# Performance work log

Measured on AMD Instinct MI355X. Metric: run time of the kernel, lower is better.

Reference implementation:

```python
import jax, jax.numpy as jnp
import numpy as np

B, C_EDGE, C_FUSED, C_SEM = 4, 64, 128, 128
H = W = 64
MASK_SIZE = 11
EPS = 1e-6


def _window_mask(h, w, mask_size):
    # M_dw: 0 inside the clipped (mask_size x mask_size) window around each query pixel, -10000 outside.
    half = mask_size // 2
    idx = jnp.arange(h * w)
    qx, qy = idx // w, idx % w
    inside = (jnp.abs(qx[:, None] - qx[None, :]) <= half) & (jnp.abs(qy[:, None] - qy[None, :]) <= half)
    return jnp.where(inside, 0.0, -10000.0).astype(jnp.float32)


def _conv1x1(x, w, b):
    # x: [b, cin, h, w], w: [cout, cin]
    return jnp.einsum('bchw,oc->bohw', x, w) + b[None, :, None, None]


def _proj1d(x, w, b):
    # x: [b, cin, n], w: [cout, cin]
    return jnp.einsum('bcn,oc->bon', x, w) + b[None, :, None]


def _bilinear(x, h, w):
    # matches F.interpolate(mode='bilinear', align_corners=False)
    b, c = x.shape[0], x.shape[1]
    return jax.image.resize(x, (b, c, h, w), method='linear', antialias=False)


def setup_inputs() -> dict:
    key = jax.random.key(0)
    ks = jax.random.split(key, 13)
    s = 0.05
    return {
        'edge_features': jax.random.normal(ks[0], (B, C_EDGE, 32, 32), jnp.float32),
        'semantic_features': jax.random.normal(ks[1], (B, C_SEM, H, W), jnp.float32),
        'fused_features': jax.random.normal(ks[2], (B, C_FUSED, 32, 32), jnp.float32),
        'w_align': jax.random.normal(ks[3], (C_SEM, C_EDGE), jnp.float32) * s,
        'b_align': jax.random.normal(ks[4], (C_SEM,), jnp.float32) * s,
        'w_fused_align': jax.random.normal(ks[5], (C_SEM, C_FUSED), jnp.float32) * s,
        'b_fused_align': jax.random.normal(ks[6], (C_SEM,), jnp.float32) * s,
        'w_q': jax.random.normal(ks[7], (2 * C_SEM, 2 * C_SEM), jnp.float32) * s,
        'b_q': jax.random.normal(ks[8], (2 * C_SEM,), jnp.float32) * s,
        'w_k': jax.random.normal(ks[9], (2 * C_SEM, 2 * C_SEM), jnp.float32) * s,
        'b_k': jax.random.normal(ks[10], (2 * C_SEM,), jnp.float32) * s,
        'w_fusion': jax.random.normal(ks[11], (C_SEM, 2 * C_SEM), jnp.float32) * s,
        'b_fusion': jax.random.normal(ks[12], (C_SEM,), jnp.float32) * s,
    }


def reference(edge_features, semantic_features, fused_features,
              w_align, b_align, w_fused_align, b_fused_align,
              w_q, b_q, w_k, b_k, w_fusion, b_fusion):
    b, c, h, w = semantic_features.shape
    n = h * w

    edge = _conv1x1(_bilinear(edge_features, h, w), w_align, b_align)            # [b,c,h,w]
    fused = _conv1x1(_bilinear(fused_features, h, w), w_fused_align, b_fused_align)

    l2_edge = jnp.sqrt(jnp.sum(edge * edge, axis=1, keepdims=True))              # [b,1,h,w]
    l2_sem = jnp.sqrt(jnp.sum(semantic_features * semantic_features, axis=1, keepdims=True))
    similarity = jnp.sum((edge / (l2_edge + EPS)) * (semantic_features / (l2_sem + EPS)),
                         axis=1, keepdims=True)
    similarity = (similarity + 1.0) * 0.5

    density_flat = l2_edge.reshape(b, n)
    density = (jax.nn.softmax(density_flat, axis=1) * n).reshape(b, 1, h, w)

    edge_t = (edge * similarity).reshape(b, c, n)
    sem_t = (semantic_features * density).reshape(b, c, n)
    fused_t = fused.reshape(b, c, n)
    sem_raw = semantic_features.reshape(b, c, n)

    edge_cat = jnp.concatenate([edge_t, edge_t], axis=1)    # [b,2c,n]
    sem_cat = jnp.concatenate([sem_t, fused_t], axis=1)
    sem_val = jnp.concatenate([sem_raw, fused_t], axis=1)

    q = _proj1d(edge_cat, w_q, b_q)                          # [b,2c,n]
    k = _proj1d(sem_cat, w_k, b_k)

    scale = 1.0 / jnp.sqrt(jnp.float32(2 * c))
    attn = jnp.einsum('bcn,bcm->bnm', q, k) * scale          # [b,n,n]
    attn = attn + _window_mask(h, w, MASK_SIZE)
    attn = jax.nn.softmax(attn, axis=-1)

    out = jnp.einsum('bnm,bcm->bnc', attn, sem_val)          # [b,n,2c]
    out = out.reshape(b, h, w, 2 * c).transpose(0, 3, 1, 2)  # [b,2c,h,w]
    return _conv1x1(out, w_fusion, b_fusion)
```

## Files before the change

### kernel.cpp

```cpp
#include <hip/hip_runtime.h>
#include <hip/hip_bf16.h>

#define NB 4
#define C 128
#define N 4096
#define EPS 1e-6f
#define PW 80
#define PIMG 5120

typedef float f32x4 __attribute__((ext_vector_type(4)));
typedef short bf16x8 __attribute__((ext_vector_type(8)));
typedef unsigned short ushort_t;
typedef unsigned int uint_t;

__device__ __forceinline__ ushort_t f2bf(float f) {
  __hip_bfloat16 h = __float2bfloat16(f);
  return *reinterpret_cast<ushort_t*>(&h);
}

struct alignas(8) us4 { ushort_t a, b, c, d; };

__device__ __forceinline__ void conv_body(const float* __restrict__ x,
                                          const float* __restrict__ w,
                                          const float* __restrict__ bias,
                                          float* __restrict__ out,
                                          int n, int o0, int b, int CIN) {
  const float* xb = x + (size_t)(b * CIN) * 1024 + n;
  float a0 = 0.f, a1 = 0.f, a2 = 0.f, a3 = 0.f;
  for (int c = 0; c < CIN; ++c) {
    float xv = xb[(size_t)c * 1024];
    a0 += w[(o0 + 0) * CIN + c] * xv;
    a1 += w[(o0 + 1) * CIN + c] * xv;
    a2 += w[(o0 + 2) * CIN + c] * xv;
    a3 += w[(o0 + 3) * CIN + c] * xv;
  }
  size_t ob = ((size_t)b * 128 + o0) * 1024 + n;
  out[ob]        = a0 + bias[o0];
  out[ob + 1024] = a1 + bias[o0 + 1];
  out[ob + 2048] = a2 + bias[o0 + 2];
  out[ob + 3072] = a3 + bias[o0 + 3];
}

__global__ void prep_misc(const float* __restrict__ edge_f, const float* __restrict__ w_align,
                          const float* __restrict__ b_align,
                          const float* __restrict__ fused_f, const float* __restrict__ w_fal,
                          const float* __restrict__ b_fal,
                          const float* __restrict__ wq, const float* __restrict__ wk,
                          const float* __restrict__ wf,
                          ushort_t* __restrict__ wqf, ushort_t* __restrict__ wkf,
                          ushort_t* __restrict__ wff,
                          float* __restrict__ edge32, float* __restrict__ fused32,
                          float* __restrict__ dsum) {
  int bx = blockIdx.x, t = threadIdx.x;
  if (bx < 64) {
    if (bx == 0 && t < NB) dsum[t] = 0.f;
    int c = bx * 256 + t;
    int lane = c & 63;
    int mrow = lane & 15, quad = lane >> 4;
    if (c < 4096) {
      int grp = c >> 6;
      int tile = grp >> 2, kslot = grp & 3;
      int o = tile * 16 + mrow, k0 = kslot * 32 + quad * 8;
      const float* s = wq + o * 256 + k0;
      ushort_t* d = wqf + (size_t)c * 8;
#pragma unroll
      for (int j = 0; j < 8; ++j) d[j] = f2bf(s[j] + s[128 + j]);
    } else if (c < 12288) {
      int c2 = c - 4096;
      int grp = c2 >> 6;
      int tile = grp >> 3, kslot = grp & 7;
      int o = tile * 16 + mrow, k0 = kslot * 32 + quad * 8;
      const float* s = wk + o * 256 + k0;
      ushort_t* d = wkf + (size_t)c2 * 8;
#pragma unroll
      for (int j = 0; j < 8; ++j) d[j] = f2bf(s[j]);
    } else {
      int c2 = c - 12288;
      int grp = c2 >> 6;
      int tile = grp >> 3, kslot = grp & 7;
      int o = tile * 16 + mrow, k0 = kslot * 32 + quad * 8;
      const float* s = wf + o * 256 + k0;
      ushort_t* d = wff + (size_t)c2 * 8;
#pragma unroll
      for (int j = 0; j < 8; ++j) d[j] = f2bf(s[j]);
    }
  } else if (bx < 576) {
    int j = bx - 64;
    conv_body(edge_f, w_align, b_align, edge32, (j & 3) * 256 + t, ((j >> 2) & 31) * 4, j >> 7, 64);
  } else {
    int j = bx - 576;
    conv_body(fused_f, w_fal, b_fal, fused32, (j & 3) * 256 + t, ((j >> 2) & 31) * 4, j >> 7, 128);
  }
}

__global__ __launch_bounds__(256) void prep_acts(const float* __restrict__ edge32,
                                                 const float* __restrict__ fused32,
                                                 const float* __restrict__ sem,
                                                 const ushort_t* __restrict__ wqf,
                                                 const ushort_t* __restrict__ wff,
                                                 const float* __restrict__ b_q,
                                                 ushort_t* __restrict__ xt_sem,
                                                 ushort_t* __restrict__ xt_fused,
                                                 float* __restrict__ simb,
                                                 float* __restrict__ l2e,
                                                 float* __restrict__ dsum,
                                                 ushort_t* __restrict__ qtb,
                                                 ushort_t* __restrict__ v2b) {
  int b = blockIdx.y, bx = blockIdx.x;
  int y = bx >> 1, xh = (bx & 1) * 32;
  int t = threadIdx.x;
  int nl = t & 31, cg = t >> 5;
  int x = xh + nl;
  int yy0 = (y & 1) ? (y >> 1) : (y >> 1) - 1;
  float fy = (y & 1) ? 0.25f : 0.75f;
  int y0c = max(yy0, 0), y1c = min(yy0 + 1, 31);
  int xx0 = (x & 1) ? (x >> 1) : (x >> 1) - 1;
  float fx = (x & 1) ? 0.25f : 0.75f;
  int x0c = max(xx0, 0), x1c = min(xx0 + 1, 31);

  __shared__ uint_t se[32][68], ssm[32][68], sf[32][68];
  __shared__ float red[4][3][32];
  __shared__ float simL[32];
  __shared__ ushort_t vstg[128 * 40];

  float ee = 0.f, ssum = 0.f, es = 0.f;
#pragma unroll 2
  for (int p = 0; p < 8; ++p) {
    float evs[2], fvs[2], svs[2];
#pragma unroll
    for (int u = 0; u < 2; ++u) {
      int c = cg * 16 + p * 2 + u;
      const float* ip = edge32 + ((size_t)(b * 128 + c)) * 1024;
      float e00 = ip[y0c * 32 + x0c], e01 = ip[y0c * 32 + x1c];
      float e10 = ip[y1c * 32 + x0c], e11 = ip[y1c * 32 + x1c];
      float ev = (1.f - fy) * ((1.f - fx) * e00 + fx * e01) + fy * ((1.f - fx) * e10 + fx * e11);
      const float* fp = fused32 + ((size_t)(b * 128 + c)) * 1024;
      float f00 = fp[y0c * 32 + x0c], f01 = fp[y0c * 32 + x1c];
      float f10 = fp[y1c * 32 + x0c], f11 = fp[y1c * 32 + x1c];
      float fv = (1.f - fy) * ((1.f - fx) * f00 + fx * f01) + fy * ((1.f - fx) * f10 + fx * f11);
      float sv = sem[((size_t)(b * 128 + c)) * 4096 + y * 64 + x];
      ee += ev * ev; ssum += sv * sv; es += ev * sv;
      evs[u] = ev; fvs[u] = fv; svs[u] = sv;
    }
    int col = cg * 8 + p;
    se[nl][col]  = (uint_t)f2bf(evs[0]) | ((uint_t)f2bf(evs[1]) << 16);
    sf[nl][col]  = (uint_t)f2bf(fvs[0]) | ((uint_t)f2bf(fvs[1]) << 16);
    ssm[nl][col] = (uint_t)f2bf(svs[0]) | ((uint_t)f2bf(svs[1]) << 16);
  }
  ee += __shfl_xor(ee, 32, 64); ssum += __shfl_xor(ssum, 32, 64); es += __shfl_xor(es, 32, 64);
  int w = t >> 6, lane = t & 63;
  int l15 = lane & 15, quad = lane >> 4;
  if (lane < 32) { red[w][0][lane] = ee; red[w][1][lane] = ssum; red[w][2][lane] = es; }
  __syncthreads();

  int base_n = b * 4096 + y * 64 + xh;
#pragma unroll
  for (int rep = 0; rep < 8; ++rep) {
    int d = rep * 256 + t;
    int r = d >> 6, cp = d & 63;
    ((uint_t*)xt_sem)[(size_t)(base_n + r) * 64 + cp] = ssm[r][cp];
    ((uint_t*)xt_fused)[(size_t)(base_n + r) * 64 + cp] = sf[r][cp];
  }
  if (t < 32) {
    float E = 0.f, S = 0.f, X = 0.f;
#pragma unroll
    for (int w2 = 0; w2 < 4; ++w2) { E += red[w2][0][t]; S += red[w2][1][t]; X += red[w2][2][t]; }
    float le = sqrtf(E), ls = sqrtf(S);
    float sv = (X / ((le + EPS) * (ls + EPS)) + 1.f) * 0.5f;
    simb[base_n + t] = sv;
    simL[t] = sv;
    l2e[base_n + t] = le;
    float pe = expf(le - 16.f);
#pragma unroll
    for (int m2 = 16; m2; m2 >>= 1) pe += __shfl_xor(pe, m2, 64);
    if (t == 0) atomicAdd(&dsum[b], pe);
  }
  __syncthreads();

#pragma unroll
  for (int h = 0; h < 2; ++h) {
    f32x4 vacc[2];
    vacc[0] = (f32x4){0.f,0.f,0.f,0.f};
    vacc[1] = (f32x4){0.f,0.f,0.f,0.f};
#pragma unroll
    for (int kk = 0; kk < 4; ++kk) {
      bf16x8 bfr = *(const bf16x8*)&ssm[h * 16 + l15][kk * 16 + quad * 4];
#pragma unroll
      for (int i = 0; i < 2; ++i) {
        bf16x8 afr = *(const bf16x8*)(wff + (size_t)(((w + i * 4) * 8 + kk) * 64 + lane) * 8);
        vacc[i] = __builtin_amdgcn_mfma_f32_16x16x32_bf16(afr, bfr, vacc[i], 0, 0, 0);
      }
    }
#pragma unroll
    for (int kk = 0; kk < 4; ++kk) {
      bf16x8 bfr = *(const bf16x8*)&sf[h * 16 + l15][kk * 16 + quad * 4];
#pragma unroll
      for (int i = 0; i < 2; ++i) {
        bf16x8 afr = *(const bf16x8*)(wff + (size_t)(((w + i * 4) * 8 + 4 + kk) * 64 + lane) * 8);
        vacc[i] = __builtin_amdgcn_mfma_f32_16x16x32_bf16(afr, bfr, vacc[i], 0, 0, 0);
      }
    }
#pragma unroll
    for (int i = 0; i < 2; ++i) {
#pragma unroll
      for (int r = 0; r < 4; ++r) {
        int ch = (w + i * 4) * 16 + quad * 4 + r;
        vstg[ch * 40 + h * 16 + l15] = f2bf(vacc[i][r]);
      }
    }
  }

#pragma unroll
  for (int h = 0; h < 2; ++h) {
    f32x4 qacc[4];
#pragma unroll
    for (int i = 0; i < 4; ++i) qacc[i] = (f32x4){0.f,0.f,0.f,0.f};
#pragma unroll
    for (int kk = 0; kk < 4; ++kk) {
      bf16x8 bfr = *(const bf16x8*)&se[h * 16 + l15][kk * 16 + quad * 4];
#pragma unroll
      for (int i = 0; i < 4; ++i) {
        bf16x8 afr = *(const bf16x8*)(wqf + (size_t)(((w * 4 + i) * 4 + kk) * 64 + lane) * 8);
        qacc[i] = __builtin_amdgcn_mfma_f32_16x16x32_bf16(afr, bfr, qacc[i], 0, 0, 0);
      }
    }
    int px = h * 16 + l15;
    float sv = simL[px];
    int n = y * 64 + xh + px;
#pragma unroll
    for (int i = 0; i < 4; ++i) {
      int o = (w * 4 + i) * 16 + quad * 4;
      float4 bq = *(const float4*)(b_q + o);
      us4 pk = { f2bf(sv * qacc[i][0] + bq.x), f2bf(sv * qacc[i][1] + bq.y),
                 f2bf(sv * qacc[i][2] + bq.z), f2bf(sv * qacc[i][3] + bq.w) };
      *(us4*)(qtb + ((size_t)b * N + n) * 256 + o) = pk;
    }
  }

  __syncthreads();
  int np0 = y * PW + 8 + xh;
#pragma unroll
  for (int r2 = 0; r2 < 2; ++r2) {
    int idx = r2 * 256 + t;
    int ch = idx >> 2, seg = idx & 3;
    *(bf16x8*)(v2b + ((size_t)b * 128 + ch) * PIMG + np0 + seg * 8) =
        *(const bf16x8*)&vstg[ch * 40 + seg * 8];
  }
}

__global__ __launch_bounds__(256) void gemm_k(const ushort_t* __restrict__ xt_sem,
                                              const ushort_t* __restrict__ xt_fused,
                                              const ushort_t* __restrict__ wkf,
                                              const float* __restrict__ b_k,
                                              const float* __restrict__ l2e,
                                              const float* __restrict__ dsum,
                                              ushort_t* __restrict__ ktb) {
  int y = blockIdx.x, bI = blockIdx.y;
  int t = threadIdx.x, w = t >> 6, lane = t & 63;
  int mrow = lane & 15, quad = lane >> 4;
  __shared__ __align__(16) ushort_t stg[16896];

  int n0 = y * 64, o0 = w * 64;
  float dscale = 4096.f / dsum[bI];
  for (int nt = 0; nt < 4; ++nt) {
    int n0t = n0 + nt * 16;
    const ushort_t* bS = xt_sem + ((size_t)bI * N + n0t + mrow) * 128 + quad * 8;
    const ushort_t* bF = xt_fused + ((size_t)bI * N + n0t + mrow) * 128 + quad * 8;
    f32x4 accL[4], accR[4];
#pragma unroll
    for (int i = 0; i < 4; ++i) { accL[i] = (f32x4){0.f,0.f,0.f,0.f}; accR[i] = (f32x4){0.f,0.f,0.f,0.f}; }
#pragma unroll
    for (int kk = 0; kk < 4; ++kk) {
      bf16x8 bfr = *(const bf16x8*)(bS + kk * 32);
#pragma unroll
      for (int i = 0; i < 4; ++i) {
        bf16x8 afr = *(const bf16x8*)(wkf + (size_t)((((w * 4 + i) * 8) + kk) * 64 + lane) * 8);
        accL[i] = __builtin_amdgcn_mfma_f32_16x16x32_bf16(afr, bfr, accL[i], 0, 0, 0);
      }
    }
#pragma unroll
    for (int kk = 0; kk < 4; ++kk) {
      bf16x8 bfr = *(const bf16x8*)(bF + kk * 32);
#pragma unroll
      for (int i = 0; i < 4; ++i) {
        bf16x8 afr = *(const bf16x8*)(wkf + (size_t)((((w * 4 + i) * 8) + 4 + kk) * 64 + lane) * 8);
        accR[i] = __builtin_amdgcn_mfma_f32_16x16x32_bf16(afr, bfr, accR[i], 0, 0, 0);
      }
    }
    int n = n0t + mrow;
    float dv = expf(l2e[bI * N + n] - 16.f) * dscale;
#pragma unroll
    for (int i = 0; i < 4; ++i) {
      int o = o0 + i * 16 + quad * 4;
      float4 bk = *(const float4*)(b_k + o);
      us4 pk = { f2bf(accL[i][0] * dv + accR[i][0] + bk.x),
                 f2bf(accL[i][1] * dv + accR[i][1] + bk.y),
                 f2bf(accL[i][2] * dv + accR[i][2] + bk.z),
                 f2bf(accL[i][3] * dv + accR[i][3] + bk.w) };
      *(us4*)&stg[(nt * 16 + mrow) * 264 + o] = pk;
    }
  }
  __syncthreads();
  int np0 = y * PW + 8;
#pragma unroll
  for (int r = 0; r < 8; ++r) {
    int cidx = r * 256 + t;
    int row = cidx >> 5, cc = cidx & 31;
    *(bf16x8*)(ktb + ((size_t)bI * PIMG + np0 + row) * 256 + cc * 8) =
        *(const bf16x8*)&stg[row * 264 + cc * 8];
  }
}

__global__ __launch_bounds__(256) void attn_kernel(const ushort_t* __restrict__ qtb,
                                                   const ushort_t* __restrict__ ktb,
                                                   const ushort_t* __restrict__ v2b,
                                                   const float* __restrict__ b_fusion,
                                                   float* __restrict__ out) {
  int L = blockIdx.x;
  int xcd = L & 7, j = L >> 3;
  int b = xcd >> 1;
  int ty0 = (((xcd & 1) << 3) + (j >> 3)) * 4;
  int tx0 = (j & 7) * 8;
  int y0 = max(ty0 - 5, 0), y1 = min(ty0 + 8, 63);
  int nh = y1 - y0 + 1;
  int x0a = tx0 - 8, cb = tx0;
  int ntq = (nh * 3 + 1) >> 1;
  int npv = (nh * 3 + 3) >> 2;

  __shared__ ushort_t pst[32][352];
  __shared__ float redm[4][2][16], reds[4][2][16];

  int t = threadIdx.x, w = t >> 6, lane = t & 63;
  int l15 = lane & 15, quad = lane >> 4;

  int gap = npv * 32 - ntq * 16;
  for (int idx = t; idx < 32 * gap; idx += 256)
    pst[idx & 31][ntq * 16 + (idx >> 5)] = 0;

  int n_s0 = (ty0 + (l15 >> 3)) * 64 + tx0 + (l15 & 7);
  int n_s1 = n_s0 + 128;
  bf16x8 qfr[2][8];
  {
    const ushort_t* q0 = qtb + ((size_t)b * N + n_s0) * 256 + quad * 8;
    const ushort_t* q1 = qtb + ((size_t)b * N + n_s1) * 256 + quad * 8;
#pragma unroll
    for (int ks = 0; ks < 8; ++ks) {
      qfr[0][ks] = *(const bf16x8*)(q0 + ks * 32);
      qfr[1][ks] = *(const bf16x8*)(q1 + ks * 32);
    }
  }
  int qx = tx0 + (l15 & 7);
  int qy0 = ty0 + (l15 >> 3);

  const ushort_t* kb = ktb + (size_t)b * PIMG * 256;
  f32x4 sc[6][2];
#pragma unroll
  for (int i = 0; i < 6; ++i) {
    int tq = w + i * 4;
    if (tq >= ntq) break;
    int key = tq * 16 + l15;
    int ry = (key * 2731) >> 16;
    int rx = key - ry * 24;
    int yy = min(y0 + ry, 63);
    const ushort_t* krow = kb + (size_t)(yy * PW + cb + rx) * 256 + quad * 8;
    f32x4 a0 = (f32x4){0.f,0.f,0.f,0.f}, a1 = (f32x4){0.f,0.f,0.f,0.f};
#pragma unroll
    for (int ks = 0; ks < 8; ++ks) {
      bf16x8 afr = *(const bf16x8*)(krow + ks * 32);
      a0 = __builtin_amdgcn_mfma_f32_16x16x32_bf16(afr, qfr[0][ks], a0, 0, 0, 0);
      a1 = __builtin_amdgcn_mfma_f32_16x16x32_bf16(afr, qfr[1][ks], a1, 0, 0, 0);
    }
    sc[i][0] = a0; sc[i][1] = a1;
  }
  float mymax0 = -1e30f, mymax1 = -1e30f;
#pragma unroll
  for (int i = 0; i < 6; ++i) {
    int tq = w + i * 4;
    if (tq >= ntq) break;
#pragma unroll
    for (int r = 0; r < 4; ++r) {
      int key = tq * 16 + quad * 4 + r;
      int ry = (key * 2731) >> 16;
      int rx = key - ry * 24;
      int x = x0a + rx;
      int dx = x - qx;
      bool xok = (dx >= -5) && (dx <= 5) && (x >= 0) && (x <= 63) && (ry < nh);
      int dy0 = y0 + ry - qy0;
      float s0 = (xok && dy0 >= -5 && dy0 <= 5) ? sc[i][0][r] * 0.0625f : -1e30f;
      int dy1 = dy0 - 2;
      float s1 = (xok && dy1 >= -5 && dy1 <= 5) ? sc[i][1][r] * 0.0625f : -1e30f;
      sc[i][0][r] = s0; sc[i][1][r] = s1;
      mymax0 = fmaxf(mymax0, s0); mymax1 = fmaxf(mymax1, s1);
    }
  }
  mymax0 = fmaxf(mymax0, __shfl_xor(mymax0, 16, 64));
  mymax0 = fmaxf(mymax0, __shfl_xor(mymax0, 32, 64));
  mymax1 = fmaxf(mymax1, __shfl_xor(mymax1, 16, 64));
  mymax1 = fmaxf(mymax1, __shfl_xor(mymax1, 32, 64));
  if (quad == 0) { redm[w][0][l15] = mymax0; redm[w][1][l15] = mymax1; }
  __syncthreads();
  float gmax0 = fmaxf(fmaxf(redm[0][0][l15], redm[1][0][l15]), fmaxf(redm[2][0][l15], redm[3][0][l15]));
  float gmax1 = fmaxf(fmaxf(redm[0][1][l15], redm[1][1][l15]), fmaxf(redm[2][1][l15], redm[3][1][l15]));
  float mysum0 = 0.f, mysum1 = 0.f;
#pragma unroll
  for (int i = 0; i < 6; ++i) {
    int tq = w + i * 4;
    if (tq >= ntq) break;
#pragma unroll
    for (int r = 0; r < 4; ++r) {
      float e0 = expf(sc[i][0][r] - gmax0);
      float e1 = expf(sc[i][1][r] - gmax1);
      sc[i][0][r] = e0; sc[i][1][r] = e1;
      mysum0 += e0; mysum1 += e1;
    }
  }
  mysum0 += __shfl_xor(mysum0, 16, 64); mysum0 += __shfl_xor(mysum0, 32, 64);
  mysum1 += __shfl_xor(mysum1, 16, 64); mysum1 += __shfl_xor(mysum1, 32, 64);
  if (quad == 0) { reds[w][0][l15] = mysum0; reds[w][1][l15] = mysum1; }
#pragma unroll
  for (int i = 0; i < 6; ++i) {
    int tq = w + i * 4;
    if (tq >= ntq) break;
    int kc = tq * 16 + quad * 4;
#pragma unroll
    for (int s = 0; s < 2; ++s) {
      uint_t p01 = (uint_t)f2bf(sc[i][s][0]) | ((uint_t)f2bf(sc[i][s][1]) << 16);
      uint_t p23 = (uint_t)f2bf(sc[i][s][2]) | ((uint_t)f2bf(sc[i][s][3]) << 16);
      *(uint_t*)(&pst[s * 16 + l15][kc]) = p01;
      *(uint_t*)(&pst[s * 16 + l15][kc + 2]) = p23;
    }
  }
  __syncthreads();

  float rinv0 = 1.f / (reds[0][0][l15] + reds[1][0][l15] + reds[2][0][l15] + reds[3][0][l15]);
  float rinv1 = 1.f / (reds[0][1][l15] + reds[1][1][l15] + reds[2][1][l15] + reds[3][1][l15]);

  const ushort_t* vb = v2b + (size_t)b * 128 * PIMG;
#pragma unroll
  for (int half = 0; half < 2; ++half) {
    int ch0 = half * 64 + w * 16;
    const ushort_t* vrow = vb + (size_t)(ch0 + l15) * PIMG;
    f32x4 acc0 = (f32x4){0.f,0.f,0.f,0.f}, acc1 = (f32x4){0.f,0.f,0.f,0.f};
    for (int ks = 0; ks < npv; ++ks) {
      int kst = ks * 32 + quad * 8;
      int ry = (kst * 2731) >> 16;
      int rxs = kst - ry * 24;
      int yy = min(y0 + ry, 63);
      bf16x8 av = *(const bf16x8*)(vrow + yy * PW + cb + rxs);
      bf16x8 bp0 = *(const bf16x8*)(&pst[l15][kst]);
      bf16x8 bp1 = *(const bf16x8*)(&pst[16 + l15][kst]);
      acc0 = __builtin_amdgcn_mfma_f32_16x16x32_bf16(av, bp0, acc0, 0, 0, 0);
      acc1 = __builtin_amdgcn_mfma_f32_16x16x32_bf16(av, bp1, acc1, 0, 0, 0);
    }
    int chg = ch0 + quad * 4;
    float4 bf4 = *(const float4*)(b_fusion + chg);
    float bfa[4] = {bf4.x, bf4.y, bf4.z, bf4.w};
#pragma unroll
    for (int r = 0; r < 4; ++r) {
      out[((size_t)b * 128 + chg + r) * N + n_s0] = acc0[r] * rinv0 + bfa[r];
      out[((size_t)b * 128 + chg + r) * N + n_s1] = acc1[r] * rinv1 + bfa[r];
    }
  }
}

extern "C" void kernel_launch(void* const* d_in, const int* in_sizes, int n_in,
                              void* d_out, int out_size, void* d_ws, size_t ws_size,
                              hipStream_t stream) {
  (void)in_sizes; (void)n_in; (void)out_size; (void)ws_size;
  const float* edge_f  = (const float*)d_in[0];
  const float* sem     = (const float*)d_in[1];
  const float* fused_f = (const float*)d_in[2];
  const float* w_align = (const float*)d_in[3];
  const float* b_align = (const float*)d_in[4];
  const float* w_fal   = (const float*)d_in[5];
  const float* b_fal   = (const float*)d_in[6];
  const float* w_q     = (const float*)d_in[7];
  const float* b_q     = (const float*)d_in[8];
  const float* w_k     = (const float*)d_in[9];
  const float* b_k     = (const float*)d_in[10];
  const float* w_fus   = (const float*)d_in[11];
  const float* b_fus   = (const float*)d_in[12];
  float* out = (float*)d_out;

  float* ws = (float*)d_ws;
  float* edge32   = ws;
  float* fused32  = ws + 524288;
  float* simb     = ws + 1048576;
  float* l2e      = ws + 1064960;
  float* dsum     = ws + 1081344;
  ushort_t* xt_sem   = (ushort_t*)(ws + 1097728);
  ushort_t* xt_fused = (ushort_t*)(ws + 2146304);
  ushort_t* wqf      = (ushort_t*)(ws + 3194880);
  ushort_t* wkf      = (ushort_t*)(ws + 3211264);
  ushort_t* wff      = (ushort_t*)(ws + 3244032);
  ushort_t* qtb      = (ushort_t*)(ws + 3260416);
  ushort_t* ktb      = (ushort_t*)(ws + 5357568);
  ushort_t* v2b      = (ushort_t*)(ws + 7979008);

  prep_misc<<<1088, 256, 0, stream>>>(edge_f, w_align, b_align, fused_f, w_fal, b_fal,
                                      w_q, w_k, w_fus, wqf, wkf, wff, edge32, fused32, dsum);
  prep_acts<<<dim3(128, NB), 256, 0, stream>>>(edge32, fused32, sem, wqf, wff, b_q,
                                               xt_sem, xt_fused, simb, l2e, dsum, qtb, v2b);
  gemm_k<<<dim3(64, NB), 256, 0, stream>>>(xt_sem, xt_fused, wkf, b_k, l2e, dsum, ktb);
  attn_kernel<<<512, 256, 0, stream>>>(qtb, ktb, v2b, b_fus, out);
}
```

Measured before the change: 159.6 us.

## Double prep_acts threads per block and split gemm_k into 16-row blocks

prep_acts now runs 512 threads per block, so each wave handles half the channels, one V tile and two Q tiles. The cross-wave reduction buffer grows to eight entries to match. gemm_k launches four times as many blocks, each computing 16 pixels instead of looping over 64, with a smaller shared staging buffer. Both changes aim to raise parallelism and occupancy on the memory-bound preparation stages, at the cost of more blocks and less weight reuse per block.

After: 159.6 us. Within noise of the previous version (+0.0%).

```diff
diff --git a/kernel.cpp b/kernel.cpp
--- a/kernel.cpp
+++ b/kernel.cpp
@@ -93,19 +93,19 @@
   }
 }
 
-__global__ __launch_bounds__(256) void prep_acts(const float* __restrict__ edge32,
-                                                 const float* __restrict__ fused32,
-                                                 const float* __restrict__ sem,
-                                                 const ushort_t* __restrict__ wqf,
-                                                 const ushort_t* __restrict__ wff,
-                                                 const float* __restrict__ b_q,
-                                                 ushort_t* __restrict__ xt_sem,
-                                                 ushort_t* __restrict__ xt_fused,
-                                                 float* __restrict__ simb,
-                                                 float* __restrict__ l2e,
-                                                 float* __restrict__ dsum,
-                                                 ushort_t* __restrict__ qtb,
-                                                 ushort_t* __restrict__ v2b) {
+__global__ __launch_bounds__(512, 4) void prep_acts(const float* __restrict__ edge32,
+                                                    const float* __restrict__ fused32,
+                                                    const float* __restrict__ sem,
+                                                    const ushort_t* __restrict__ wqf,
+                                                    const ushort_t* __restrict__ wff,
+                                                    const float* __restrict__ b_q,
+                                                    ushort_t* __restrict__ xt_sem,
+                                                    ushort_t* __restrict__ xt_fused,
+                                                    float* __restrict__ simb,
+                                                    float* __restrict__ l2e,
+                                                    float* __restrict__ dsum,
+                                                    ushort_t* __restrict__ qtb,
+                                                    ushort_t* __restrict__ v2b) {
   int b = blockIdx.y, bx = blockIdx.x;
   int y = bx >> 1, xh = (bx & 1) * 32;
   int t = threadIdx.x;
@@ -119,17 +119,17 @@
   int x0c = max(xx0, 0), x1c = min(xx0 + 1, 31);
 
   __shared__ uint_t se[32][68], ssm[32][68], sf[32][68];
-  __shared__ float red[4][3][32];
+  __shared__ float red[8][3][32];
   __shared__ float simL[32];
   __shared__ ushort_t vstg[128 * 40];
 
   float ee = 0.f, ssum = 0.f, es = 0.f;
 #pragma unroll 2
-  for (int p = 0; p < 8; ++p) {
+  for (int p = 0; p < 4; ++p) {
     float evs[2], fvs[2], svs[2];
 #pragma unroll
     for (int u = 0; u < 2; ++u) {
-      int c = cg * 16 + p * 2 + u;
+      int c = cg * 8 + p * 2 + u;
       const float* ip = edge32 + ((size_t)(b * 128 + c)) * 1024;
       float e00 = ip[y0c * 32 + x0c], e01 = ip[y0c * 32 + x1c];
       float e10 = ip[y1c * 32 + x0c], e11 = ip[y1c * 32 + x1c];
@@ -142,7 +142,7 @@
       ee += ev * ev; ssum += sv * sv; es += ev * sv;
       evs[u] = ev; fvs[u] = fv; svs[u] = sv;
     }
-    int col = cg * 8 + p;
+    int col = cg * 4 + p;
     se[nl][col]  = (uint_t)f2bf(evs[0]) | ((uint_t)f2bf(evs[1]) << 16);
     sf[nl][col]  = (uint_t)f2bf(fvs[0]) | ((uint_t)f2bf(fvs[1]) << 16);
     ssm[nl][col] = (uint_t)f2bf(svs[0]) | ((uint_t)f2bf(svs[1]) << 16);
@@ -155,8 +155,8 @@
 
   int base_n = b * 4096 + y * 64 + xh;
 #pragma unroll
-  for (int rep = 0; rep < 8; ++rep) {
-    int d = rep * 256 + t;
+  for (int rep = 0; rep < 4; ++rep) {
+    int d = rep * 512 + t;
     int r = d >> 6, cp = d & 63;
     ((uint_t*)xt_sem)[(size_t)(base_n + r) * 64 + cp] = ssm[r][cp];
     ((uint_t*)xt_fused)[(size_t)(base_n + r) * 64 + cp] = sf[r][cp];
@@ -164,7 +164,7 @@
   if (t < 32) {
     float E = 0.f, S = 0.f, X = 0.f;
 #pragma unroll
-    for (int w2 = 0; w2 < 4; ++w2) { E += red[w2][0][t]; S += red[w2][1][t]; X += red[w2][2][t]; }
+    for (int w2 = 0; w2 < 8; ++w2) { E += red[w2][0][t]; S += red[w2][1][t]; X += red[w2][2][t]; }
     float le = sqrtf(E), ls = sqrtf(S);
     float sv = (X / ((le + EPS) * (ls + EPS)) + 1.f) * 0.5f;
     simb[base_n + t] = sv;
@@ -179,48 +179,37 @@
 
 #pragma unroll
   for (int h = 0; h < 2; ++h) {
-    f32x4 vacc[2];
-    vacc[0] = (f32x4){0.f,0.f,0.f,0.f};
-    vacc[1] = (f32x4){0.f,0.f,0.f,0.f};
+    f32x4 vacc = (f32x4){0.f,0.f,0.f,0.f};
 #pragma unroll
     for (int kk = 0; kk < 4; ++kk) {
       bf16x8 bfr = *(const bf16x8*)&ssm[h * 16 + l15][kk * 16 + quad * 4];
-#pragma unroll
-      for (int i = 0; i < 2; ++i) {
-        bf16x8 afr = *(const bf16x8*)(wff + (size_t)(((w + i * 4) * 8 + kk) * 64 + lane) * 8);
-        vacc[i] = __builtin_amdgcn_mfma_f32_16x16x32_bf16(afr, bfr, vacc[i], 0, 0, 0);
-      }
+      bf16x8 afr = *(const bf16x8*)(wff + (size_t)((w * 8 + kk) * 64 + lane) * 8);
+      vacc = __builtin_amdgcn_mfma_f32_16x16x32_bf16(afr, bfr, vacc, 0, 0, 0);
     }
 #pragma unroll
     for (int kk = 0; kk < 4; ++kk) {
       bf16x8 bfr = *(const bf16x8*)&sf[h * 16 + l15][kk * 16 + quad * 4];
-#pragma unroll
-      for (int i = 0; i < 2; ++i) {
-        bf16x8 afr = *(const bf16x8*)(wff + (size_t)(((w + i * 4) * 8 + 4 + kk) * 64 + lane) * 8);
-        vacc[i] = __builtin_amdgcn_mfma_f32_16x16x32_bf16(afr, bfr, vacc[i], 0, 0, 0);
-      }
-    }
-#pragma unroll
-    for (int i = 0; i < 2; ++i) {
-#pragma unroll
-      for (int r = 0; r < 4; ++r) {
-        int ch = (w + i * 4) * 16 + quad * 4 + r;
-        vstg[ch * 40 + h * 16 + l15] = f2bf(vacc[i][r]);
-      }
+      bf16x8 afr = *(const bf16x8*)(wff + (size_t)((w * 8 + 4 + kk) * 64 + lane) * 8);
+      vacc = __builtin_amdgcn_mfma_f32_16x16x32_bf16(afr, bfr, vacc, 0, 0, 0);
+    }
+#pragma unroll
+    for (int r = 0; r < 4; ++r) {
+      int ch = w * 16 + quad * 4 + r;
+      vstg[ch * 40 + h * 16 + l15] = f2bf(vacc[r]);
     }
   }
 
 #pragma unroll
   for (int h = 0; h < 2; ++h) {
-    f32x4 qacc[4];
-#pragma unroll
-    for (int i = 0; i < 4; ++i) qacc[i] = (f32x4){0.f,0.f,0.f,0.f};
+    f32x4 qacc[2];
+#pragma unroll
+    for (int i = 0; i < 2; ++i) qacc[i] = (f32x4){0.f,0.f,0.f,0.f};
 #pragma unroll
     for (int kk = 0; kk < 4; ++kk) {
       bf16x8 bfr = *(const bf16x8*)&se[h * 16 + l15][kk * 16 + quad * 4];
 #pragma unroll
-      for (int i = 0; i < 4; ++i) {
-        bf16x8 afr = *(const bf16x8*)(wqf + (size_t)(((w * 4 + i) * 4 + kk) * 64 + lane) * 8);
+      for (int i = 0; i < 2; ++i) {
+        bf16x8 afr = *(const bf16x8*)(wqf + (size_t)(((w * 2 + i) * 4 + kk) * 64 + lane) * 8);
         qacc[i] = __builtin_amdgcn_mfma_f32_16x16x32_bf16(afr, bfr, qacc[i], 0, 0, 0);
       }
     }
@@ -228,8 +217,8 @@
     float sv = simL[px];
     int n = y * 64 + xh + px;
 #pragma unroll
-    for (int i = 0; i < 4; ++i) {
-      int o = (w * 4 + i) * 16 + quad * 4;
+    for (int i = 0; i < 2; ++i) {
+      int o = (w * 2 + i) * 16 + quad * 4;
       float4 bq = *(const float4*)(b_q + o);
       us4 pk = { f2bf(sv * qacc[i][0] + bq.x), f2bf(sv * qacc[i][1] + bq.y),
                  f2bf(sv * qacc[i][2] + bq.z), f2bf(sv * qacc[i][3] + bq.w) };
@@ -239,71 +228,66 @@
 
   __syncthreads();
   int np0 = y * PW + 8 + xh;
-#pragma unroll
-  for (int r2 = 0; r2 < 2; ++r2) {
-    int idx = r2 * 256 + t;
-    int ch = idx >> 2, seg = idx & 3;
+  {
+    int ch = t >> 2, seg = t & 3;
     *(bf16x8*)(v2b + ((size_t)b * 128 + ch) * PIMG + np0 + seg * 8) =
         *(const bf16x8*)&vstg[ch * 40 + seg * 8];
   }
 }
 
-__global__ __launch_bounds__(256) void gemm_k(const ushort_t* __restrict__ xt_sem,
-                                              const ushort_t* __restrict__ xt_fused,
-                                              const ushort_t* __restrict__ wkf,
-                                              const float* __restrict__ b_k,
-                                              const float* __restrict__ l2e,
-                                              const float* __restrict__ dsum,
-                                              ushort_t* __restrict__ ktb) {
-  int y = blockIdx.x, bI = blockIdx.y;
+__global__ __launch_bounds__(256, 4) void gemm_k(const ushort_t* __restrict__ xt_sem,
+                                                 const ushort_t* __restrict__ xt_fused,
+                                                 const ushort_t* __restrict__ wkf,
+                                                 const float* __restrict__ b_k,
+                                                 const float* __restrict__ l2e,
+                                                 const float* __restrict__ dsum,
+                                                 ushort_t* __restrict__ ktb) {
+  int bx = blockIdx.x, bI = blockIdx.y;
   int t = threadIdx.x, w = t >> 6, lane = t & 63;
   int mrow = lane & 15, quad = lane >> 4;
-  __shared__ __align__(16) ushort_t stg[16896];
-
-  int n0 = y * 64, o0 = w * 64;
+  __shared__ __align__(16) ushort_t stg[16 * 264];
+
+  int n0 = bx * 16, o0 = w * 64;
   float dscale = 4096.f / dsum[bI];
-  for (int nt = 0; nt < 4; ++nt) {
-    int n0t = n0 + nt * 16;
-    const ushort_t* bS = xt_sem + ((size_t)bI * N + n0t + mrow) * 128 + quad * 8;
-    const ushort_t* bF = xt_fused + ((size_t)bI * N + n0t + mrow) * 128 + quad * 8;
-    f32x4 accL[4], accR[4];
-#pragma unroll
-    for (int i = 0; i < 4; ++i) { accL[i] = (f32x4){0.f,0.f,0.f,0.f}; accR[i] = (f32x4){0.f,0.f,0.f,0.f}; }
-#pragma unroll
-    for (int kk = 0; kk < 4; ++kk) {
-      bf16x8 bfr = *(const bf16x8*)(bS + kk * 32);
-#pragma unroll
-      for (int i = 0; i < 4; ++i) {
-        bf16x8 afr = *(const bf16x8*)(wkf + (size_t)((((w * 4 + i) * 8) + kk) * 64 + lane) * 8);
-        accL[i] = __builtin_amdgcn_mfma_f32_16x16x32_bf16(afr, bfr, accL[i], 0, 0, 0);
-      }
-    }
-#pragma unroll
-    for (int kk = 0; kk < 4; ++kk) {
-      bf16x8 bfr = *(const bf16x8*)(bF + kk * 32);
-#pragma unroll
-      for (int i = 0; i < 4; ++i) {
-        bf16x8 afr = *(const bf16x8*)(wkf + (size_t)((((w * 4 + i) * 8) + 4 + kk) * 64 + lane) * 8);
-        accR[i] = __builtin_amdgcn_mfma_f32_16x16x32_bf16(afr, bfr, accR[i], 0, 0, 0);
-      }
-    }
-    int n = n0t + mrow;
-    float dv = expf(l2e[bI * N + n] - 16.f) * dscale;
+  const ushort_t* bS = xt_sem + ((size_t)bI * N + n0 + mrow) * 128 + quad * 8;
+  const ushort_t* bF = xt_fused + ((size_t)bI * N + n0 + mrow) * 128 + quad * 8;
+  f32x4 accL[4], accR[4];
+#pragma unroll
+  for (int i = 0; i < 4; ++i) { accL[i] = (f32x4){0.f,0.f,0.f,0.f}; accR[i] = (f32x4){0.f,0.f,0.f,0.f}; }
+#pragma unroll
+  for (int kk = 0; kk < 4; ++kk) {
+    bf16x8 bfr = *(const bf16x8*)(bS + kk * 32);
 #pragma unroll
     for (int i = 0; i < 4; ++i) {
-      int o = o0 + i * 16 + quad * 4;
-      float4 bk = *(const float4*)(b_k + o);
-      us4 pk = { f2bf(accL[i][0] * dv + accR[i][0] + bk.x),
-                 f2bf(accL[i][1] * dv + accR[i][1] + bk.y),
-                 f2bf(accL[i][2] * dv + accR[i][2] + bk.z),
-                 f2bf(accL[i][3] * dv + accR[i][3] + bk.w) };
-      *(us4*)&stg[(nt * 16 + mrow) * 264 + o] = pk;
-    }
-  }
-  __syncthreads();
-  int np0 = y * PW + 8;
-#pragma unroll
-  for (int r = 0; r < 8; ++r) {
+      bf16x8 afr = *(const bf16x8*)(wkf + (size_t)((((w * 4 + i) * 8) + kk) * 64 + lane) * 8);
+      accL[i] = __builtin_amdgcn_mfma_f32_16x16x32_bf16(afr, bfr, accL[i], 0, 0, 0);
+    }
+  }
+#pragma unroll
+  for (int kk = 0; kk < 4; ++kk) {
+    bf16x8 bfr = *(const bf16x8*)(bF + kk * 32);
+#pragma unroll
+    for (int i = 0; i < 4; ++i) {
+      bf16x8 afr = *(const bf16x8*)(wkf + (size_t)((((w * 4 + i) * 8) + 4 + kk) * 64 + lane) * 8);
+      accR[i] = __builtin_amdgcn_mfma_f32_16x16x32_bf16(afr, bfr, accR[i], 0, 0, 0);
+    }
+  }
+  int n = n0 + mrow;
+  float dv = expf(l2e[bI * N + n] - 16.f) * dscale;
+#pragma unroll
+  for (int i = 0; i < 4; ++i) {
+    int o = o0 + i * 16 + quad * 4;
+    float4 bk = *(const float4*)(b_k + o);
+    us4 pk = { f2bf(accL[i][0] * dv + accR[i][0] + bk.x),
+               f2bf(accL[i][1] * dv + accR[i][1] + bk.y),
+               f2bf(accL[i][2] * dv + accR[i][2] + bk.z),
+               f2bf(accL[i][3] * dv + accR[i][3] + bk.w) };
+    *(us4*)&stg[mrow * 264 + o] = pk;
+  }
+  __syncthreads();
+  int np0 = (n0 >> 6) * PW + 8 + (n0 & 63);
+#pragma unroll
+  for (int r = 0; r < 2; ++r) {
     int cidx = r * 256 + t;
     int row = cidx >> 5, cc = cidx & 31;
     *(bf16x8*)(ktb + ((size_t)bI * PIMG + np0 + row) * 256 + cc * 8) =
@@ -499,8 +483,8 @@
 
   prep_misc<<<1088, 256, 0, stream>>>(edge_f, w_align, b_align, fused_f, w_fal, b_fal,
                                       w_q, w_k, w_fus, wqf, wkf, wff, edge32, fused32, dsum);
-  prep_acts<<<dim3(128, NB), 256, 0, stream>>>(edge32, fused32, sem, wqf, wff, b_q,
+  prep_acts<<<dim3(128, NB), 512, 0, stream>>>(edge32, fused32, sem, wqf, wff, b_q,
                                                xt_sem, xt_fused, simb, l2e, dsum, qtb, v2b);
-  gemm_k<<<dim3(64, NB), 256, 0, stream>>>(xt_sem, xt_fused, wkf, b_k, l2e, dsum, ktb);
+  gemm_k<<<dim3(256, NB), 256, 0, stream>>>(xt_sem, xt_fused, wkf, b_k, l2e, dsum, ktb);
   attn_kernel<<<512, 256, 0, stream>>>(qtb, ktb, v2b, b_fus, out);
 }
```
